# Performance work log

Measured on AMD Instinct MI355X. Metric: run time of the kernel, lower is better.

Reference implementation:

```python
import jax, jax.numpy as jnp
import numpy as np

EPS = 0.1  # eps added to covariance sums, as in torch cov()
N, D, N_CLASSES = 4096, 1024, 64


def setup_inputs() -> dict:
    key = jax.random.key(0)
    k1, k2 = jax.random.split(key)
    inputs = jax.random.normal(k1, (N, D), dtype=jnp.float32)
    targets = jax.random.randint(k2, (N,), 0, N_CLASSES, dtype=jnp.int32)
    return {"inputs": inputs, "targets": targets}


def _masked_sqdiff_sum(M, x):
    # Per-dim sum over masked pairs (i,j) of (x_i - x_j)^2, without
    # materializing the [n, n, d] difference tensor:
    #   sum_ij M_ij (x_id^2 + x_jd^2 - 2 x_id x_jd)
    row = M.sum(axis=1)  # [n]
    col = M.sum(axis=0)  # [n]
    x2 = x * x
    return row @ x2 + col @ x2 - 2.0 * jnp.sum(x * (M @ x), axis=0)  # [d]


def _jeffrey_loss(inputs, targets):
    n = inputs.shape[0]
    same = targets[:, None] == targets[None, :]
    eye = jnp.eye(n, dtype=bool)
    pos_m = (same & ~eye).astype(inputs.dtype)  # positive pairs, i != j
    neg_m = (~same).astype(inputs.dtype)        # negative pairs

    # Covariances are computed on detached diffs in the torch code
    xd = jax.lax.stop_gradient(inputs)
    cnt_pos = pos_m.sum()
    cnt_neg = neg_m.sum()
    sigma1 = (_masked_sqdiff_sum(pos_m, xd) + EPS) / cnt_pos  # [d]
    sigma0 = (_masked_sqdiff_sum(neg_m, xd) + EPS) / cnt_neg  # [d]
    weights = 1.0 / sigma0 - 1.0 / sigma1  # [d], constant w.r.t. grad

    # S[i, j] = sum_d weights_d * (x_i - x_j)_d^2, via gram expansion
    xw = inputs * weights            # [n, d]
    sq = jnp.sum(inputs * xw, axis=1)  # [n], sum_d w_d x_d^2
    S = sq[:, None] + sq[None, :] - 2.0 * inputs @ xw.T  # [n, n]

    # BCEWithLogitsLoss(mean): label 1 on positive pairs (logits a),
    # label 0 on negative pairs (logits b)
    loss_sum = jnp.sum(pos_m * jax.nn.softplus(-S)) + jnp.sum(neg_m * jax.nn.softplus(S))
    return loss_sum / (cnt_pos + cnt_neg)


def reference(inputs, targets):
    return _jeffrey_loss(inputs, targets)
```

## Files before the change

### kernel.cpp

```cpp
#include <hip/hip_runtime.h>
#include <stdint.h>

#define N_ROWS 4096
#define DIM    1024
#define NCLS   64
#define EPSV   0.1f

typedef __attribute__((ext_vector_type(8))) __bf16 bf16x8;
typedef __attribute__((ext_vector_type(4))) float  f32x4;

__device__ __forceinline__ unsigned short f2bf(float f) {
    union { float f; unsigned u; } v; v.f = f;
    unsigned r = v.u + 0x7FFF + ((v.u >> 16) & 1);
    return (unsigned short)(r >> 16);
}

__device__ __forceinline__ void async_cp16(const void* g, void* l) {
    __builtin_amdgcn_global_load_lds((const __attribute__((address_space(1))) void*)g,
                                     (__attribute__((address_space(3))) void*)l,
                                     16, 0, 0);
}

__device__ __forceinline__ float softplus(float x) {
    return fmaxf(x, 0.f) + __logf(1.f + __expf(-fabsf(x)));
}

__global__ __launch_bounds__(256) void k_cstats(const float* __restrict__ X,
                                                const int* __restrict__ tgt,
                                                float* __restrict__ csumR,
                                                float* __restrict__ csqR) {
    __shared__ int rows[N_ROWS];
    __shared__ int nrows_s;
    int tid = threadIdx.x;
    int c = blockIdx.x >> 2, q = blockIdx.x & 3;
    if (tid == 0) nrows_s = 0;
    __syncthreads();
    for (int i = tid; i < N_ROWS; i += 256)
        if (tgt[i] == c) { int p = atomicAdd(&nrows_s, 1); rows[p] = i; }
    __syncthreads();
    int n = nrows_s;
    int d = q * 256 + tid;
    float s = 0.f, qq = 0.f;
    #pragma unroll 4
    for (int r = 0; r < n; r++) {
        float x = X[(size_t)rows[r] * DIM + d];
        s += x; qq += x * x;
    }
    csumR[c * DIM + d] = s;
    csqR [c * DIM + d] = qq;
}

__global__ __launch_bounds__(256) void k_weights(const int* __restrict__ tgt,
                                                 const float* __restrict__ csumR,
                                                 const float* __restrict__ csqR,
                                                 float* __restrict__ w,
                                                 float* __restrict__ loss_out) {
    __shared__ int hist[NCLS];
    int tid = threadIdx.x;
    if (tid < NCLS) hist[tid] = 0;
    __syncthreads();
    for (int i = tid; i < N_ROWS; i += 256) atomicAdd(&hist[tgt[i]], 1);
    __syncthreads();
    float cnt_pos, cnt_neg;
    {
        long long sp = 0, ss = 0;
        for (int c = 0; c < NCLS; c++) { long long cc = hist[c]; sp += cc * (cc - 1); ss += cc * cc; }
        cnt_pos = (float)sp;
        cnt_neg = (float)((long long)N_ROWS * N_ROWS - ss);
    }
    int d = blockIdx.x * 256 + tid;
    float A = 0.f, X2 = 0.f, T = 0.f, SS = 0.f;
    #pragma unroll 8
    for (int c = 0; c < NCLS; c++) {
        float s = csumR[c * DIM + d];
        float q = csqR [c * DIM + d];
        A += (float)hist[c] * q; X2 += q; T += s; SS += s * s;
    }
    float posnum = 2.f * (A - SS);
    float negnum = 2.f * ((float)N_ROWS * X2 - A - T * T + SS);
    w[d] = cnt_neg / (negnum + EPSV) - cnt_pos / (posnum + EPSV);
    if (blockIdx.x == 0 && tid == 0) loss_out[0] = 0.0f;
}

__global__ __launch_bounds__(256) void k_prep(const float* __restrict__ X,
                                              const float* __restrict__ w,
                                              unsigned short* __restrict__ Xb,
                                              unsigned short* __restrict__ XWb,
                                              float* __restrict__ sq) {
    int row = blockIdx.x, tid = threadIdx.x;
    const float4* xr = (const float4*)(X + (size_t)row * DIM);
    const float4* wr = (const float4*)w;
    float4 x = xr[tid], ww = wr[tid];
    float4 xw = make_float4(x.x * ww.x, x.y * ww.y, x.z * ww.z, x.w * ww.w);
    float p = x.x * xw.x + x.y * xw.y + x.z * xw.z + x.w * xw.w;
    ushort4 xb, xwb;
    xb.x  = f2bf(x.x);  xb.y  = f2bf(x.y);  xb.z  = f2bf(x.z);  xb.w  = f2bf(x.w);
    xwb.x = f2bf(xw.x); xwb.y = f2bf(xw.y); xwb.z = f2bf(xw.z); xwb.w = f2bf(xw.w);
    ((ushort4*)(Xb  + (size_t)row * DIM))[tid] = xb;
    ((ushort4*)(XWb + (size_t)row * DIM))[tid] = xwb;
    for (int off = 32; off; off >>= 1) p += __shfl_down(p, off, 64);
    __shared__ float red[4];
    int wv = tid >> 6, ln = tid & 63;
    if (ln == 0) red[wv] = p;
    __syncthreads();
    if (tid == 0) sq[row] = red[0] + red[1] + red[2] + red[3];
}

__global__ __launch_bounds__(512) void k_gemm_loss(const unsigned short* __restrict__ Xb,
                                                   const unsigned short* __restrict__ XWb,
                                                   const float* __restrict__ sq,
                                                   const int* __restrict__ tgt,
                                                   float* __restrict__ loss) {
    __shared__ __align__(16) unsigned short As[4][128 * 32];
    __shared__ __align__(16) unsigned short Bs[4][128 * 32];
    __shared__ float sqI[128], sqJ[128];
    __shared__ int   tIs[128], tJs[128];
    __shared__ float red[8];

    int tid = threadIdx.x;
    int wave = tid >> 6, lane = tid & 63;

    int g = blockIdx.x & 7, s = blockIdx.x >> 3;
    int sz0 = g + 1, sz1 = g + 9, sz2 = g + 17, sz3 = g + 25;
    int jt, it;
    if      (s < sz0)             { jt = g;      it = s; }
    else if (s < sz0 + sz1)       { jt = g + 8;  it = s - sz0; }
    else if (s < sz0 + sz1 + sz2) { jt = g + 16; it = s - sz0 - sz1; }
    else if (s < sz0 + sz1 + sz2 + sz3) { jt = g + 24; it = s - sz0 - sz1 - sz2; }
    else return;

    const unsigned short* gp[2];
    unsigned short* lb[2];
    #pragma unroll
    for (int si = 0; si < 2; si++) {
        int gI = wave * 2 + si;
        int R  = gI * 16 + (lane >> 2);
        int q  = (lane & 3) ^ ((R >> 1) & 3);
        int r  = R & 127;
        bool isA = R < 128;
        int grow = (isA ? it : jt) * 128 + r;
        const unsigned short* src = isA ? Xb : XWb;
        gp[si] = src + (size_t)grow * DIM + q * 8;
        lb[si] = (isA ? &As[0][0] : &Bs[0][0]) + (gI & 7) * (16 * 32);
    }

    int lr = lane & 15, kq = lane >> 4;
    int offA[4], offB[2];
    int wrow = (wave >> 2) * 64, wcol = (wave & 3) * 32;
    #pragma unroll
    for (int mi = 0; mi < 4; mi++) {
        int row = wrow + mi * 16 + lr;
        offA[mi] = row * 32 + (kq ^ ((row >> 1) & 3)) * 8;
    }
    #pragma unroll
    for (int nj = 0; nj < 2; nj++) {
        int col = wcol + nj * 16 + lr;
        offB[nj] = col * 32 + (kq ^ ((col >> 1) & 3)) * 8;
    }

    f32x4 acc[4][2];
    #pragma unroll
    for (int i = 0; i < 4; i++)
        #pragma unroll
        for (int j = 0; j < 2; j++) acc[i][j] = (f32x4){0.f, 0.f, 0.f, 0.f};

    #pragma unroll
    for (int st = 0; st < 3; st++)
        #pragma unroll
        for (int si = 0; si < 2; si++)
            async_cp16(gp[si] + st * 32, lb[si] + st * (128 * 32));

    for (int kk = 0; kk < 32; kk++) {
        if      (kk < 30)  asm volatile("s_waitcnt vmcnt(4)" ::: "memory");
        else if (kk == 30) asm volatile("s_waitcnt vmcnt(2)" ::: "memory");
        else               asm volatile("s_waitcnt vmcnt(0)" ::: "memory");
        asm volatile("s_barrier" ::: "memory");
        if (kk < 29) {
            int wr = (kk + 3) & 3;
            #pragma unroll
            for (int si = 0; si < 2; si++)
                async_cp16(gp[si] + (kk + 3) * 32, lb[si] + wr * (128 * 32));
        }
        int rd = kk & 3;
        const unsigned short* Ab = As[rd];
        const unsigned short* Bb = Bs[rd];
        bf16x8 av[4], bv[2];
        #pragma unroll
        for (int i = 0; i < 4; i++) av[i] = *(const bf16x8*)(Ab + offA[i]);
        #pragma unroll
        for (int j = 0; j < 2; j++) bv[j] = *(const bf16x8*)(Bb + offB[j]);
        #pragma unroll
        for (int i = 0; i < 4; i++)
            #pragma unroll
            for (int j = 0; j < 2; j++)
                acc[i][j] = __builtin_amdgcn_mfma_f32_16x16x32_bf16(av[i], bv[j], acc[i][j], 0, 0, 0);
    }

    __syncthreads();
    if (tid < 128)      { sqI[tid] = sq[it * 128 + tid]; tIs[tid] = tgt[it * 128 + tid]; }
    else if (tid < 256) { int u = tid - 128; sqJ[u] = sq[jt * 128 + u]; tJs[u] = tgt[jt * 128 + u]; }
    __syncthreads();

    float sum = 0.f;
    bool diagTile = (it == jt);
    #pragma unroll
    for (int j = 0; j < 2; j++) {
        int col = wcol + j * 16 + (lane & 15);
        float sj = sqJ[col]; int tj = tJs[col];
        #pragma unroll
        for (int i = 0; i < 4; i++) {
            int rbase = wrow + i * 16 + (lane >> 4) * 4;
            #pragma unroll
            for (int r = 0; r < 4; r++) {
                int rowp = rbase + r;
                float S = sqI[rowp] + sj - 2.f * acc[i][j][r];
                float v;
                if (tIs[rowp] == tj) v = (diagTile && rowp == col) ? 0.f : softplus(-S);
                else                 v = softplus(S);
                sum += v;
            }
        }
    }
    float scale = (diagTile ? 1.f : 2.f) * (1.f / ((float)N_ROWS * (float)(N_ROWS - 1)));
    sum *= scale;
    for (int off = 32; off; off >>= 1) sum += __shfl_down(sum, off, 64);
    if (lane == 0) red[wave] = sum;
    __syncthreads();
    if (tid == 0) {
        float t = 0.f;
        #pragma unroll
        for (int wv = 0; wv < 8; wv++) t += red[wv];
        atomicAdd(loss, t);
    }
}

extern "C" void kernel_launch(void* const* d_in, const int* in_sizes, int n_in,
                              void* d_out, int out_size, void* d_ws, size_t ws_size,
                              hipStream_t stream) {
    const float* X  = (const float*)d_in[0];
    const int* tgt  = (const int*)d_in[1];
    float* out = (float*)d_out;
    char* ws = (char*)d_ws;
    const size_t MB = 1u << 20;

    float* w        = (float*)ws;
    float* sq       = (float*)(ws + 4096);
    unsigned short* Xb  = (unsigned short*)(ws + 1 * MB);
    unsigned short* XWb = (unsigned short*)(ws + 9 * MB);
    float* csumR    = (float*)(ws + 17 * MB);
    float* csqR     = (float*)(ws + 17 * MB + 256 * 1024);

    k_cstats  <<<256,  256, 0, stream>>>(X, tgt, csumR, csqR);
    k_weights <<<4,    256, 0, stream>>>(tgt, csumR, csqR, w, out);
    k_prep    <<<4096, 256, 0, stream>>>(X, w, Xb, XWb, sq);
    k_gemm_loss<<<640, 512, 0, stream>>>(Xb, XWb, sq, tgt, out);
}
```

Baseline: 127.9 us.

## Switch Gram GEMM to FP8 MFMA with power-of-two scaling of weighted operand

Quantizes X and X*w to FP8 instead of BF16 and runs the Gram matrix on 16x16x32 FP8 MFMA, halving operand bytes and K-loop LDS/global traffic. A single-block weights kernel computes an RMS-based power-of-two scale for X*w so it fits FP8 range, and the epilogue rescales the dot product. The tile schedule is rebalanced to pair column tiles (g, 15-g, ...) and the grid shrinks to 528 blocks with no early-exit blocks. FP8 precision loss in the pairwise distances S may change the loss beyond tolerance.

```diff
diff --git a/kernel.cpp b/kernel.cpp
--- a/kernel.cpp
+++ b/kernel.cpp
@@ -6,14 +6,7 @@
 #define NCLS   64
 #define EPSV   0.1f
 
-typedef __attribute__((ext_vector_type(8))) __bf16 bf16x8;
-typedef __attribute__((ext_vector_type(4))) float  f32x4;
-
-__device__ __forceinline__ unsigned short f2bf(float f) {
-    union { float f; unsigned u; } v; v.f = f;
-    unsigned r = v.u + 0x7FFF + ((v.u >> 16) & 1);
-    return (unsigned short)(r >> 16);
-}
+typedef __attribute__((ext_vector_type(4))) float f32x4;
 
 __device__ __forceinline__ void async_cp16(const void* g, void* l) {
     __builtin_amdgcn_global_load_lds((const __attribute__((address_space(1))) void*)g,
@@ -50,25 +43,24 @@
     csqR [c * DIM + d] = qq;
 }
 
-__global__ __launch_bounds__(256) void k_weights(const int* __restrict__ tgt,
-                                                 const float* __restrict__ csumR,
-                                                 const float* __restrict__ csqR,
-                                                 float* __restrict__ w,
-                                                 float* __restrict__ loss_out) {
+__global__ __launch_bounds__(1024) void k_weights(const int* __restrict__ tgt,
+                                                  const float* __restrict__ csumR,
+                                                  const float* __restrict__ csqR,
+                                                  float* __restrict__ w,
+                                                  float* __restrict__ scal,
+                                                  float* __restrict__ loss_out) {
     __shared__ int hist[NCLS];
+    __shared__ float redw[16];
     int tid = threadIdx.x;
     if (tid < NCLS) hist[tid] = 0;
     __syncthreads();
-    for (int i = tid; i < N_ROWS; i += 256) atomicAdd(&hist[tgt[i]], 1);
-    __syncthreads();
-    float cnt_pos, cnt_neg;
-    {
-        long long sp = 0, ss = 0;
-        for (int c = 0; c < NCLS; c++) { long long cc = hist[c]; sp += cc * (cc - 1); ss += cc * cc; }
-        cnt_pos = (float)sp;
-        cnt_neg = (float)((long long)N_ROWS * N_ROWS - ss);
-    }
-    int d = blockIdx.x * 256 + tid;
+    for (int i = tid; i < N_ROWS; i += 1024) atomicAdd(&hist[tgt[i]], 1);
+    __syncthreads();
+    long long sp = 0, ss = 0;
+    for (int c = 0; c < NCLS; c++) { long long cc = hist[c]; sp += cc * (cc - 1); ss += cc * cc; }
+    float cnt_pos = (float)sp;
+    float cnt_neg = (float)((long long)N_ROWS * N_ROWS - ss);
+    int d = tid;
     float A = 0.f, X2 = 0.f, T = 0.f, SS = 0.f;
     #pragma unroll 8
     for (int c = 0; c < NCLS; c++) {
@@ -78,26 +70,42 @@
     }
     float posnum = 2.f * (A - SS);
     float negnum = 2.f * ((float)N_ROWS * X2 - A - T * T + SS);
-    w[d] = cnt_neg / (negnum + EPSV) - cnt_pos / (posnum + EPSV);
-    if (blockIdx.x == 0 && tid == 0) loss_out[0] = 0.0f;
+    float wd = cnt_neg / (negnum + EPSV) - cnt_pos / (posnum + EPSV);
+    w[d] = wd;
+    float m = wd * wd;
+    for (int off = 32; off; off >>= 1) m += __shfl_down(m, off, 64);
+    int wv = tid >> 6, ln = tid & 63;
+    if (ln == 0) redw[wv] = m;
+    __syncthreads();
+    if (tid == 0) {
+        float ms = 0.f;
+        #pragma unroll
+        for (int i = 0; i < 16; i++) ms += redw[i];
+        ms /= 1024.f;
+        float sw = exp2f(roundf(log2f(sqrtf(ms) + 1e-30f)));
+        scal[0] = sw;
+        loss_out[0] = 0.0f;
+    }
 }
 
 __global__ __launch_bounds__(256) void k_prep(const float* __restrict__ X,
                                               const float* __restrict__ w,
-                                              unsigned short* __restrict__ Xb,
-                                              unsigned short* __restrict__ XWb,
+                                              const float* __restrict__ scal,
+                                              unsigned int* __restrict__ Xb8,
+                                              unsigned int* __restrict__ XWb8,
                                               float* __restrict__ sq) {
     int row = blockIdx.x, tid = threadIdx.x;
-    const float4* xr = (const float4*)(X + (size_t)row * DIM);
-    const float4* wr = (const float4*)w;
-    float4 x = xr[tid], ww = wr[tid];
+    float inv_sw = 1.0f / scal[0];
+    float4 x  = ((const float4*)(X + (size_t)row * DIM))[tid];
+    float4 ww = ((const float4*)w)[tid];
     float4 xw = make_float4(x.x * ww.x, x.y * ww.y, x.z * ww.z, x.w * ww.w);
     float p = x.x * xw.x + x.y * xw.y + x.z * xw.z + x.w * xw.w;
-    ushort4 xb, xwb;
-    xb.x  = f2bf(x.x);  xb.y  = f2bf(x.y);  xb.z  = f2bf(x.z);  xb.w  = f2bf(x.w);
-    xwb.x = f2bf(xw.x); xwb.y = f2bf(xw.y); xwb.z = f2bf(xw.z); xwb.w = f2bf(xw.w);
-    ((ushort4*)(Xb  + (size_t)row * DIM))[tid] = xb;
-    ((ushort4*)(XWb + (size_t)row * DIM))[tid] = xwb;
+    unsigned ux = __builtin_amdgcn_cvt_pk_fp8_f32(x.x, x.y, 0, false);
+    ux = __builtin_amdgcn_cvt_pk_fp8_f32(x.z, x.w, ux, true);
+    unsigned uw = __builtin_amdgcn_cvt_pk_fp8_f32(xw.x * inv_sw, xw.y * inv_sw, 0, false);
+    uw = __builtin_amdgcn_cvt_pk_fp8_f32(xw.z * inv_sw, xw.w * inv_sw, uw, true);
+    Xb8 [row * 256 + tid] = ux;
+    XWb8[row * 256 + tid] = uw;
     for (int off = 32; off; off >>= 1) p += __shfl_down(p, off, 64);
     __shared__ float red[4];
     int wv = tid >> 6, ln = tid & 63;
@@ -106,13 +114,14 @@
     if (tid == 0) sq[row] = red[0] + red[1] + red[2] + red[3];
 }
 
-__global__ __launch_bounds__(512) void k_gemm_loss(const unsigned short* __restrict__ Xb,
-                                                   const unsigned short* __restrict__ XWb,
+__global__ __launch_bounds__(512) void k_gemm_loss(const unsigned char* __restrict__ Xb8,
+                                                   const unsigned char* __restrict__ XWb8,
                                                    const float* __restrict__ sq,
                                                    const int* __restrict__ tgt,
+                                                   const float* __restrict__ scal,
                                                    float* __restrict__ loss) {
-    __shared__ __align__(16) unsigned short As[4][128 * 32];
-    __shared__ __align__(16) unsigned short Bs[4][128 * 32];
+    __shared__ __align__(16) unsigned char As[4][128 * 32];
+    __shared__ __align__(16) unsigned char Bs[4][128 * 32];
     __shared__ float sqI[128], sqJ[128];
     __shared__ int   tIs[128], tJs[128];
     __shared__ float red[8];
@@ -121,28 +130,22 @@
     int wave = tid >> 6, lane = tid & 63;
 
     int g = blockIdx.x & 7, s = blockIdx.x >> 3;
-    int sz0 = g + 1, sz1 = g + 9, sz2 = g + 17, sz3 = g + 25;
+    int j0 = g, j1 = 15 - g, j2 = 16 + g, j3 = 31 - g;
+    int n0 = j0 + 1, n1 = j1 + 1, n2 = j2 + 1;
     int jt, it;
-    if      (s < sz0)             { jt = g;      it = s; }
-    else if (s < sz0 + sz1)       { jt = g + 8;  it = s - sz0; }
-    else if (s < sz0 + sz1 + sz2) { jt = g + 16; it = s - sz0 - sz1; }
-    else if (s < sz0 + sz1 + sz2 + sz3) { jt = g + 24; it = s - sz0 - sz1 - sz2; }
-    else return;
-
-    const unsigned short* gp[2];
-    unsigned short* lb[2];
-    #pragma unroll
-    for (int si = 0; si < 2; si++) {
-        int gI = wave * 2 + si;
-        int R  = gI * 16 + (lane >> 2);
-        int q  = (lane & 3) ^ ((R >> 1) & 3);
-        int r  = R & 127;
-        bool isA = R < 128;
-        int grow = (isA ? it : jt) * 128 + r;
-        const unsigned short* src = isA ? Xb : XWb;
-        gp[si] = src + (size_t)grow * DIM + q * 8;
-        lb[si] = (isA ? &As[0][0] : &Bs[0][0]) + (gI & 7) * (16 * 32);
-    }
+    if      (s < n0)           { jt = j0; it = s; }
+    else if (s < n0 + n1)      { jt = j1; it = s - n0; }
+    else if (s < n0 + n1 + n2) { jt = j2; it = s - n0 - n1; }
+    else                       { jt = j3; it = s - n0 - n1 - n2; }
+
+    bool isA = wave < 4;
+    int gIa = wave & 3;
+    int r_loc = gIa * 32 + (lane >> 1);
+    int swb = ((r_loc >> 1) ^ (r_loc >> 2)) & 1;
+    int h_src = (lane & 1) ^ swb;
+    int grow = (isA ? it : jt) * 128 + r_loc;
+    const unsigned char* gp = (isA ? Xb8 : XWb8) + (size_t)grow * DIM + h_src * 16;
+    unsigned char* lbase = (isA ? &As[0][0] : &Bs[0][0]) + gIa * 1024;
 
     int lr = lane & 15, kq = lane >> 4;
     int offA[4], offB[2];
@@ -150,12 +153,12 @@
     #pragma unroll
     for (int mi = 0; mi < 4; mi++) {
         int row = wrow + mi * 16 + lr;
-        offA[mi] = row * 32 + (kq ^ ((row >> 1) & 3)) * 8;
+        offA[mi] = row * 32 + ((kq ^ ((((row >> 1) ^ (row >> 2)) & 1) << 1)) * 8);
     }
     #pragma unroll
     for (int nj = 0; nj < 2; nj++) {
         int col = wcol + nj * 16 + lr;
-        offB[nj] = col * 32 + (kq ^ ((col >> 1) & 3)) * 8;
+        offB[nj] = col * 32 + ((kq ^ ((((col >> 1) ^ (col >> 2)) & 1) << 1)) * 8);
     }
 
     f32x4 acc[4][2];
@@ -165,35 +168,29 @@
         for (int j = 0; j < 2; j++) acc[i][j] = (f32x4){0.f, 0.f, 0.f, 0.f};
 
     #pragma unroll
-    for (int st = 0; st < 3; st++)
-        #pragma unroll
-        for (int si = 0; si < 2; si++)
-            async_cp16(gp[si] + st * 32, lb[si] + st * (128 * 32));
+    for (int st = 0; st < 3; st++) async_cp16(gp + st * 32, lbase + st * (128 * 32));
 
     for (int kk = 0; kk < 32; kk++) {
-        if      (kk < 30)  asm volatile("s_waitcnt vmcnt(4)" ::: "memory");
-        else if (kk == 30) asm volatile("s_waitcnt vmcnt(2)" ::: "memory");
+        if      (kk < 30)  asm volatile("s_waitcnt vmcnt(2)" ::: "memory");
+        else if (kk == 30) asm volatile("s_waitcnt vmcnt(1)" ::: "memory");
         else               asm volatile("s_waitcnt vmcnt(0)" ::: "memory");
         asm volatile("s_barrier" ::: "memory");
         if (kk < 29) {
-            int wr = (kk + 3) & 3;
-            #pragma unroll
-            for (int si = 0; si < 2; si++)
-                async_cp16(gp[si] + (kk + 3) * 32, lb[si] + wr * (128 * 32));
+            async_cp16(gp + (kk + 3) * 32, lbase + ((kk + 3) & 3) * (128 * 32));
         }
         int rd = kk & 3;
-        const unsigned short* Ab = As[rd];
-        const unsigned short* Bb = Bs[rd];
-        bf16x8 av[4], bv[2];
-        #pragma unroll
-        for (int i = 0; i < 4; i++) av[i] = *(const bf16x8*)(Ab + offA[i]);
-        #pragma unroll
-        for (int j = 0; j < 2; j++) bv[j] = *(const bf16x8*)(Bb + offB[j]);
+        const unsigned char* Ab = As[rd];
+        const unsigned char* Bb = Bs[rd];
+        long long av[4], bv[2];
+        #pragma unroll
+        for (int i = 0; i < 4; i++) av[i] = *(const long long*)(Ab + offA[i]);
+        #pragma unroll
+        for (int j = 0; j < 2; j++) bv[j] = *(const long long*)(Bb + offB[j]);
         #pragma unroll
         for (int i = 0; i < 4; i++)
             #pragma unroll
             for (int j = 0; j < 2; j++)
-                acc[i][j] = __builtin_amdgcn_mfma_f32_16x16x32_bf16(av[i], bv[j], acc[i][j], 0, 0, 0);
+                acc[i][j] = __builtin_amdgcn_mfma_f32_16x16x32_fp8_fp8(av[i], bv[j], acc[i][j], 0, 0, 0);
     }
 
     __syncthreads();
@@ -201,6 +198,7 @@
     else if (tid < 256) { int u = tid - 128; sqJ[u] = sq[jt * 128 + u]; tJs[u] = tgt[jt * 128 + u]; }
     __syncthreads();
 
+    float sw2 = 2.0f * scal[0];
     float sum = 0.f;
     bool diagTile = (it == jt);
     #pragma unroll
@@ -213,7 +211,7 @@
             #pragma unroll
             for (int r = 0; r < 4; r++) {
                 int rowp = rbase + r;
-                float S = sqI[rowp] + sj - 2.f * acc[i][j][r];
+                float S = sqI[rowp] + sj - sw2 * acc[i][j][r];
                 float v;
                 if (tIs[rowp] == tj) v = (diagTile && rowp == col) ? 0.f : softplus(-S);
                 else                 v = softplus(S);
@@ -243,15 +241,17 @@
     char* ws = (char*)d_ws;
     const size_t MB = 1u << 20;
 
-    float* w        = (float*)ws;
-    float* sq       = (float*)(ws + 4096);
-    unsigned short* Xb  = (unsigned short*)(ws + 1 * MB);
-    unsigned short* XWb = (unsigned short*)(ws + 9 * MB);
-    float* csumR    = (float*)(ws + 17 * MB);
-    float* csqR     = (float*)(ws + 17 * MB + 256 * 1024);
+    float* w      = (float*)ws;
+    float* sq     = (float*)(ws + 4096);
+    float* scal   = (float*)(ws + 24576);
+    unsigned int* Xb8  = (unsigned int*)(ws + 1 * MB);
+    unsigned int* XWb8 = (unsigned int*)(ws + 5 * MB);
+    float* csumR  = (float*)(ws + 9 * MB);
+    float* csqR   = (float*)(ws + 9 * MB + 256 * 1024);
 
     k_cstats  <<<256,  256, 0, stream>>>(X, tgt, csumR, csqR);
-    k_weights <<<4,    256, 0, stream>>>(tgt, csumR, csqR, w, out);
-    k_prep    <<<4096, 256, 0, stream>>>(X, w, Xb, XWb, sq);
-    k_gemm_loss<<<640, 512, 0, stream>>>(Xb, XWb, sq, tgt, out);
-}
+    k_weights <<<1,   1024, 0, stream>>>(tgt, csumR, csqR, w, scal, out);
+    k_prep    <<<4096, 256, 0, stream>>>(X, w, scal, Xb8, XWb8, sq);
+    k_gemm_loss<<<528, 512, 0, stream>>>((const unsigned char*)Xb8, (const unsigned char*)XWb8,
+                                         sq, tgt, scal, out);
+}
```

Result: faster. 125.2 us (-2.1%).
